# Performance work log

Measured on AMD Instinct MI355X. Metric: run time of the kernel, lower is better.

## Reference

```python
import jax, jax.numpy as jnp
import numpy as np
from jax import lax

B, T, D = 8, 2048, 1024


def setup_inputs() -> dict:
    key = jax.random.key(0)
    ks = jax.random.split(key, 8)
    s = 1.0 / np.sqrt(D)
    x = jax.random.normal(ks[0], (B, T, D), dtype=jnp.float32)
    Wq = jax.random.uniform(ks[1], (D, D), jnp.float32, -s, s)
    bq = jax.random.uniform(ks[2], (D,), jnp.float32, -s, s)
    Wk = jax.random.uniform(ks[3], (D, D), jnp.float32, -s, s)
    bk = jax.random.uniform(ks[4], (D,), jnp.float32, -s, s)
    Wv = jax.random.uniform(ks[5], (D, D), jnp.float32, -s, s)
    bv = jax.random.uniform(ks[6], (D,), jnp.float32, -s, s)
    decay = jnp.full((D,), 0.9, dtype=jnp.float32)  # nn.Parameter(ones*0.9)
    return {"x": x, "Wq": Wq, "bq": bq, "Wk": Wk, "bk": bk,
            "Wv": Wv, "bv": bv, "decay": decay}


def reference(x, Wq, bq, Wk, bk, Wv, bv, decay):
    # projections (torch Linear: x @ W.T + b)
    q = jnp.einsum('btd,ed->bte', x, Wq) + bq
    k = jnp.einsum('btd,ed->bte', x, Wk) + bk
    v = jnp.einsum('btd,ed->bte', x, Wv) + bv
    kv = k * v  # [B,T,D]

    # diagonal-decay linear recurrence: mem_t = decay * mem_{t-1} + kv_t
    def step(mem, kv_t):
        mem = decay * mem + kv_t  # [B,D]
        return mem, mem

    mem0 = jnp.zeros((B, D), dtype=x.dtype)
    _, mems = lax.scan(step, mem0, jnp.swapaxes(kv, 0, 1))  # mems: [T,B,D]
    out = q * jnp.swapaxes(mems, 0, 1)  # output_t = q_t * mem_t
    return out
```

## Files before the change

### kernel.cpp

```cpp
#include <hip/hip_runtime.h>
#include <cstdint>

typedef unsigned short ushort_t;
typedef __bf16 bf16x8 __attribute__((ext_vector_type(8)));
typedef float f32x4 __attribute__((ext_vector_type(4)));

#define B_ 8
#define T_ 2048
#define D_ 1024
#define M_ (B_ * T_)
#define NCHUNK 64
#define CHUNKLEN 32

__device__ __forceinline__ ushort_t f2bf(float f) {
    union { float f; uint32_t u; } v; v.f = f;
    uint32_t u = v.u;
    uint32_t r = (u + 0x7fffu + ((u >> 16) & 1u)) >> 16;
    return (ushort_t)r;
}
__device__ __forceinline__ float bf2f(ushort_t h) {
    union { uint32_t u; float f; } v; v.u = ((uint32_t)h) << 16;
    return v.f;
}

__device__ __forceinline__ void async16(const ushort_t* g, ushort_t* l) {
    __builtin_amdgcn_global_load_lds(
        (const __attribute__((address_space(1))) void*)g,
        (__attribute__((address_space(3))) void*)l, 16, 0, 0);
}

__global__ __launch_bounds__(256) void cast_all(
    const float* __restrict__ x, const float* __restrict__ wq,
    const float* __restrict__ wk, const float* __restrict__ wv,
    ushort_t* __restrict__ xb, ushort_t* __restrict__ Wb) {
    const int nx4 = M_ * D_ / 4, nw4 = D_ * D_ / 4;
    int i = blockIdx.x * blockDim.x + threadIdx.x;
    const float* src; ushort_t* dstp; int si;
    if (i < nx4) {
        src = x; si = i; dstp = xb + (size_t)i * 4;
    } else {
        int j = i - nx4;
        dstp = Wb + (size_t)j * 4;
        if (j < nw4)          { src = wq; si = j; }
        else if (j < 2 * nw4) { src = wk; si = j - nw4; }
        else                  { src = wv; si = j - 2 * nw4; }
    }
    float4 v = ((const float4*)src)[si];
    ushort4 o;
    o.x = f2bf(v.x); o.y = f2bf(v.y); o.z = f2bf(v.z); o.w = f2bf(v.w);
    *(ushort4*)dstp = o;
}

__global__ __launch_bounds__(256, 2) void gemm_qkv(
    const ushort_t* __restrict__ xb, const ushort_t* __restrict__ Wq,
    const ushort_t* __restrict__ Wk, const ushort_t* __restrict__ Wv,
    const float* __restrict__ bq, const float* __restrict__ bk,
    const float* __restrict__ bv, const float* __restrict__ decay,
    ushort_t* __restrict__ qb, ushort_t* __restrict__ kvb,
    float* __restrict__ S) {
    __shared__ ushort_t As[128 * 64];
    __shared__ ushort_t B0[128 * 64];
    __shared__ ushort_t B1[128 * 64];

    const int idx = blockIdx.x;
    const bool qmode = idx < 512;
    int mb, n0;
    const ushort_t *W0, *W1;
    if (qmode) {
        mb = idx & 127; n0 = (idx >> 7) * 256;
        W0 = Wq + (size_t)n0 * D_;
        W1 = Wq + (size_t)(n0 + 128) * D_;
    } else {
        const int j = idx - 512;
        mb = j & 127; n0 = (j >> 7) * 128;
        W0 = Wk + (size_t)n0 * D_;
        W1 = Wv + (size_t)n0 * D_;
    }
    const int m0 = mb * 128;

    const int t = threadIdx.x;
    const int lane = t & 63, wv = t >> 6;
    const int wr = (wv >> 1) * 64, wc = (wv & 1) * 64;

    f32x4 acc0[4][4], acc1[4][4];
#pragma unroll
    for (int i = 0; i < 4; ++i)
#pragma unroll
        for (int j = 0; j < 4; ++j) {
            acc0[i][j] = (f32x4){0.f, 0.f, 0.f, 0.f};
            acc1[i][j] = (f32x4){0.f, 0.f, 0.f, 0.f};
        }

    const int rs = t >> 3;
    const int g = (t & 7) ^ (rs & 7);
    const int scol = g * 8;

    const int quad = lane >> 4;
    const int l7 = lane & 7;
    const int cs0 = ((quad) ^ l7) * 8;
    const int cs1 = ((4 + quad) ^ l7) * 8;
    const int rowa = wr + (lane & 15);
    const int rowb = wc + (lane & 15);

    for (int kt = 0; kt < 16; ++kt) {
        const int k0 = kt * 64;
#pragma unroll
        for (int p = 0; p < 4; ++p) {
            const int rp = rs + p * 32;
            const int Lofs = (t + p * 256) * 8;
            async16(xb + (size_t)(m0 + rp) * D_ + k0 + scol, &As[Lofs]);
            async16(W0 + (size_t)rp * D_ + k0 + scol, &B0[Lofs]);
            async16(W1 + (size_t)rp * D_ + k0 + scol, &B1[Lofs]);
        }
        __syncthreads();

#pragma unroll
        for (int h = 0; h < 2; ++h) {
            const int cs = h ? cs1 : cs0;
            bf16x8 af[4], b08[4], b18[4];
#pragma unroll
            for (int i = 0; i < 4; ++i)
                af[i] = *(const bf16x8*)&As[(rowa + i * 16) * 64 + cs];
#pragma unroll
            for (int j = 0; j < 4; ++j) {
                b08[j] = *(const bf16x8*)&B0[(rowb + j * 16) * 64 + cs];
                b18[j] = *(const bf16x8*)&B1[(rowb + j * 16) * 64 + cs];
            }
#pragma unroll
            for (int i = 0; i < 4; ++i)
#pragma unroll
                for (int j = 0; j < 4; ++j) {
                    acc0[i][j] = __builtin_amdgcn_mfma_f32_16x16x32_bf16(
                        af[i], b08[j], acc0[i][j], 0, 0, 0);
                    acc1[i][j] = __builtin_amdgcn_mfma_f32_16x16x32_bf16(
                        af[i], b18[j], acc1[i][j], 0, 0, 0);
                }
        }
        __syncthreads();
    }

    const int colq = lane & 15;
    const int rowq = quad * 4;

    if (qmode) {
        const float* bias0 = bq + n0;
        const float* bias1 = bq + n0 + 128;
#pragma unroll
        for (int i = 0; i < 4; ++i) {
#pragma unroll
            for (int j = 0; j < 4; ++j) {
                const int c = wc + j * 16 + colq;
                const float bv0 = bias0[c], bv1 = bias1[c];
#pragma unroll
                for (int r = 0; r < 4; ++r) {
                    const int rg = m0 + wr + i * 16 + rowq + r;
                    qb[(size_t)rg * D_ + n0 + c]       = f2bf(acc0[i][j][r] + bv0);
                    qb[(size_t)rg * D_ + n0 + 128 + c] = f2bf(acc1[i][j][r] + bv1);
                }
            }
        }
    } else {
        const float* bias0 = bk + n0;
        const float* bias1 = bv + n0;
        const int bidx = m0 >> 11;
        const int cbase = ((m0 & 2047) >> 5) + (wr >> 5);
        int cj[4];
        float bv0a[4], bv1a[4], d1a[4], d2a[4], d3a[4], P0a[4], P1a[4];
#pragma unroll
        for (int j = 0; j < 4; ++j) {
            const int c = wc + j * 16 + colq;
            cj[j] = c;
            bv0a[j] = bias0[c];
            bv1a[j] = bias1[c];
            const float dec = decay[n0 + c];
            const float d2 = dec * dec, d4 = d2 * d2;
            const float d8 = d4 * d4, d16 = d8 * d8;
            d1a[j] = dec; d2a[j] = d2; d3a[j] = d2 * dec;
            const float P1 = (quad == 0) ? (d8 * d4) : ((quad == 1) ? d8 : ((quad == 2) ? d4 : 1.0f));
            P1a[j] = P1;
            P0a[j] = d16 * P1;
        }
        float s0[4], s1[4];
#pragma unroll
        for (int j = 0; j < 4; ++j) { s0[j] = 0.f; s1[j] = 0.f; }

#pragma unroll
        for (int i = 0; i < 4; ++i) {
#pragma unroll
            for (int r = 0; r < 4; ++r) {
                const int rg = m0 + wr + i * 16 + rowq + r;
                ushort_t* rowp = kvb + (size_t)rg * D_ + n0;
#pragma unroll
                for (int j = 0; j < 4; ++j) {
                    const float kf = acc0[i][j][r] + bv0a[j];
                    const float vf = acc1[i][j][r] + bv1a[j];
                    const float kvf = kf * vf;
                    rowp[cj[j]] = f2bf(kvf);
                    const float w3 = (r == 0) ? d3a[j] : ((r == 1) ? d2a[j] : ((r == 2) ? d1a[j] : 1.0f));
                    const float wgt = ((i & 1) ? P1a[j] : P0a[j]) * w3;
                    if (i < 2) s0[j] = fmaf(kvf, wgt, s0[j]);
                    else       s1[j] = fmaf(kvf, wgt, s1[j]);
                }
            }
        }
#pragma unroll
        for (int j = 0; j < 4; ++j) {
            s0[j] += __shfl_xor(s0[j], 16, 64);
            s0[j] += __shfl_xor(s0[j], 32, 64);
            s1[j] += __shfl_xor(s1[j], 16, 64);
            s1[j] += __shfl_xor(s1[j], 32, 64);
        }
        if (quad == 0) {
#pragma unroll
            for (int j = 0; j < 4; ++j) {
                const int cg = n0 + cj[j];
                S[(((size_t)bidx * NCHUNK) + cbase) * D_ + cg]     = s0[j];
                S[(((size_t)bidx * NCHUNK) + cbase + 1) * D_ + cg] = s1[j];
            }
        }
    }
}

__global__ __launch_bounds__(256) void scan_final2(
    const ushort_t* __restrict__ kvb, const ushort_t* __restrict__ qb,
    const float* __restrict__ decay, const float* __restrict__ S,
    float* __restrict__ out) {
    const int b = blockIdx.x >> 6;
    const int c = blockIdx.x & 63;
    const int d0 = threadIdx.x * 4;
    const float4 dc = *(const float4*)&decay[d0];
    float e0 = dc.x, e1 = dc.y, e2 = dc.z, e3 = dc.w;
#pragma unroll
    for (int s = 0; s < 5; ++s) { e0 *= e0; e1 *= e1; e2 *= e2; e3 *= e3; }
    float m0 = 0.f, m1 = 0.f, m2 = 0.f, m3 = 0.f;
    const float* Sb = &S[((size_t)b * NCHUNK) * D_ + d0];
    for (int cc = 0; cc < c; ++cc) {
        float4 s4 = *(const float4*)&Sb[(size_t)cc * D_];
        m0 = fmaf(e0, m0, s4.x);
        m1 = fmaf(e1, m1, s4.y);
        m2 = fmaf(e2, m2, s4.z);
        m3 = fmaf(e3, m3, s4.w);
    }
    size_t base = ((size_t)b * T_ + c * CHUNKLEN) * D_ + d0;
#pragma unroll 8
    for (int i = 0; i < CHUNKLEN; ++i) {
        const size_t o = base + (size_t)i * D_;
        ushort4 kv = *(const ushort4*)&kvb[o];
        ushort4 q4 = *(const ushort4*)&qb[o];
        m0 = fmaf(dc.x, m0, bf2f(kv.x));
        m1 = fmaf(dc.y, m1, bf2f(kv.y));
        m2 = fmaf(dc.z, m2, bf2f(kv.z));
        m3 = fmaf(dc.w, m3, bf2f(kv.w));
        *(float4*)&out[o] = make_float4(bf2f(q4.x) * m0, bf2f(q4.y) * m1,
                                        bf2f(q4.z) * m2, bf2f(q4.w) * m3);
    }
}

extern "C" void kernel_launch(void* const* d_in, const int* in_sizes, int n_in,
                              void* d_out, int out_size, void* d_ws, size_t ws_size,
                              hipStream_t stream) {
    const float* x     = (const float*)d_in[0];
    const float* Wq    = (const float*)d_in[1];
    const float* bq    = (const float*)d_in[2];
    const float* Wk    = (const float*)d_in[3];
    const float* bk    = (const float*)d_in[4];
    const float* Wv    = (const float*)d_in[5];
    const float* bv    = (const float*)d_in[6];
    const float* decay = (const float*)d_in[7];
    float* out = (float*)d_out;

    char* ws = (char*)d_ws;
    ushort_t* xb  = (ushort_t*)(ws);
    ushort_t* Wb  = (ushort_t*)(ws + 33554432);
    ushort_t* qb  = (ushort_t*)(ws + 39845888);
    ushort_t* kvb = (ushort_t*)(ws + 73400320);
    float*    S   = (float*)(ws + 106954752);

    ushort_t* Wqb = Wb;
    ushort_t* Wkb = Wb + D_ * D_;
    ushort_t* Wvb = Wb + 2 * D_ * D_;

    const int ncast = (M_ * D_ / 4) + (3 * D_ * D_ / 4);
    cast_all<<<ncast / 256, 256, 0, stream>>>(x, Wq, Wk, Wv, xb, Wb);

    gemm_qkv<<<1536, 256, 0, stream>>>(xb, Wqb, Wkb, Wvb, bq, bk, bv, decay,
                                       qb, kvb, S);

    scan_final2<<<B_ * NCHUNK, 256, 0, stream>>>(kvb, qb, decay, S, out);
}
```

Baseline: 257.3 us.

## Double-buffer GEMM LDS tiles with K=32 stages and split scan over more blocks

The QKV GEMM now uses two LDS buffers of K=32 tiles, issuing async loads for the next tile while MFMAs run on the current one. This hides global-to-LDS latency and drops one barrier per step, with a new swizzle for the narrower rows. The final scan kernel splits D across two blocks per (batch, chunk), doubling the grid to 1024 blocks with 2 elements per thread. That raises occupancy and parallelism for the memory-bound output pass, at the cost of narrower vector accesses.

Measured after the change: 302.0 us. 17.4% more time.

```diff
diff --git a/kernel.cpp b/kernel.cpp
--- a/kernel.cpp
+++ b/kernel.cpp
@@ -58,9 +58,9 @@
     const float* __restrict__ bv, const float* __restrict__ decay,
     ushort_t* __restrict__ qb, ushort_t* __restrict__ kvb,
     float* __restrict__ S) {
-    __shared__ ushort_t As[128 * 64];
-    __shared__ ushort_t B0[128 * 64];
-    __shared__ ushort_t B1[128 * 64];
+    __shared__ ushort_t As[2][128 * 32];
+    __shared__ ushort_t B0[2][128 * 32];
+    __shared__ ushort_t B1[2][128 * 32];
 
     const int idx = blockIdx.x;
     const bool qmode = idx < 512;
@@ -91,53 +91,58 @@
             acc1[i][j] = (f32x4){0.f, 0.f, 0.f, 0.f};
         }
 
-    const int rs = t >> 3;
-    const int g = (t & 7) ^ (rs & 7);
+    const int rs = t >> 2;
+    const int g = (t & 3) ^ ((t >> 3) & 3);
     const int scol = g * 8;
 
     const int quad = lane >> 4;
-    const int l7 = lane & 7;
-    const int cs0 = ((quad) ^ l7) * 8;
-    const int cs1 = ((4 + quad) ^ l7) * 8;
+    const int rsw = ((lane & 15) >> 1) & 3;
+    const int cs = (quad ^ rsw) * 8;
     const int rowa = wr + (lane & 15);
     const int rowb = wc + (lane & 15);
 
-    for (int kt = 0; kt < 16; ++kt) {
-        const int k0 = kt * 64;
-#pragma unroll
-        for (int p = 0; p < 4; ++p) {
-            const int rp = rs + p * 32;
-            const int Lofs = (t + p * 256) * 8;
-            async16(xb + (size_t)(m0 + rp) * D_ + k0 + scol, &As[Lofs]);
-            async16(W0 + (size_t)rp * D_ + k0 + scol, &B0[Lofs]);
-            async16(W1 + (size_t)rp * D_ + k0 + scol, &B1[Lofs]);
-        }
+#define STAGE(bufi, ktv)                                                     \
+    do {                                                                     \
+        const int k0s = (ktv) * 32;                                          \
+        _Pragma("unroll")                                                    \
+        for (int p = 0; p < 2; ++p) {                                        \
+            const int rp = rs + p * 64;                                      \
+            const int Lofs = (t + p * 256) * 8;                              \
+            async16(xb + (size_t)(m0 + rp) * D_ + k0s + scol,                \
+                    &As[bufi][Lofs]);                                        \
+            async16(W0 + (size_t)rp * D_ + k0s + scol, &B0[bufi][Lofs]);     \
+            async16(W1 + (size_t)rp * D_ + k0s + scol, &B1[bufi][Lofs]);     \
+        }                                                                    \
+    } while (0)
+
+    STAGE(0, 0);
+    __syncthreads();
+
+    for (int kt = 0; kt < 32; ++kt) {
+        const int cur = kt & 1;
+        if (kt < 31) STAGE(cur ^ 1, kt + 1);
+
+        bf16x8 af[4], b08[4], b18[4];
+#pragma unroll
+        for (int i = 0; i < 4; ++i)
+            af[i] = *(const bf16x8*)&As[cur][(rowa + i * 16) * 32 + cs];
+#pragma unroll
+        for (int j = 0; j < 4; ++j) {
+            b08[j] = *(const bf16x8*)&B0[cur][(rowb + j * 16) * 32 + cs];
+            b18[j] = *(const bf16x8*)&B1[cur][(rowb + j * 16) * 32 + cs];
+        }
+#pragma unroll
+        for (int i = 0; i < 4; ++i)
+#pragma unroll
+            for (int j = 0; j < 4; ++j) {
+                acc0[i][j] = __builtin_amdgcn_mfma_f32_16x16x32_bf16(
+                    af[i], b08[j], acc0[i][j], 0, 0, 0);
+                acc1[i][j] = __builtin_amdgcn_mfma_f32_16x16x32_bf16(
+                    af[i], b18[j], acc1[i][j], 0, 0, 0);
+            }
         __syncthreads();
-
-#pragma unroll
-        for (int h = 0; h < 2; ++h) {
-            const int cs = h ? cs1 : cs0;
-            bf16x8 af[4], b08[4], b18[4];
-#pragma unroll
-            for (int i = 0; i < 4; ++i)
-                af[i] = *(const bf16x8*)&As[(rowa + i * 16) * 64 + cs];
-#pragma unroll
-            for (int j = 0; j < 4; ++j) {
-                b08[j] = *(const bf16x8*)&B0[(rowb + j * 16) * 64 + cs];
-                b18[j] = *(const bf16x8*)&B1[(rowb + j * 16) * 64 + cs];
-            }
-#pragma unroll
-            for (int i = 0; i < 4; ++i)
-#pragma unroll
-                for (int j = 0; j < 4; ++j) {
-                    acc0[i][j] = __builtin_amdgcn_mfma_f32_16x16x32_bf16(
-                        af[i], b08[j], acc0[i][j], 0, 0, 0);
-                    acc1[i][j] = __builtin_amdgcn_mfma_f32_16x16x32_bf16(
-                        af[i], b18[j], acc1[i][j], 0, 0, 0);
-                }
-        }
-        __syncthreads();
-    }
+    }
+#undef STAGE
 
     const int colq = lane & 15;
     const int rowq = quad * 4;
@@ -225,34 +230,31 @@
     const ushort_t* __restrict__ kvb, const ushort_t* __restrict__ qb,
     const float* __restrict__ decay, const float* __restrict__ S,
     float* __restrict__ out) {
-    const int b = blockIdx.x >> 6;
-    const int c = blockIdx.x & 63;
-    const int d0 = threadIdx.x * 4;
-    const float4 dc = *(const float4*)&decay[d0];
-    float e0 = dc.x, e1 = dc.y, e2 = dc.z, e3 = dc.w;
-#pragma unroll
-    for (int s = 0; s < 5; ++s) { e0 *= e0; e1 *= e1; e2 *= e2; e3 *= e3; }
-    float m0 = 0.f, m1 = 0.f, m2 = 0.f, m3 = 0.f;
+    const int bid = blockIdx.x;
+    const int b = bid >> 7;
+    const int c = (bid >> 1) & 63;
+    const int dh = bid & 1;
+    const int d0 = dh * 512 + threadIdx.x * 2;
+    const float2 dc2 = *(const float2*)&decay[d0];
+    float e0 = dc2.x, e1 = dc2.y;
+#pragma unroll
+    for (int s = 0; s < 5; ++s) { e0 *= e0; e1 *= e1; }
+    float m0 = 0.f, m1 = 0.f;
     const float* Sb = &S[((size_t)b * NCHUNK) * D_ + d0];
     for (int cc = 0; cc < c; ++cc) {
-        float4 s4 = *(const float4*)&Sb[(size_t)cc * D_];
-        m0 = fmaf(e0, m0, s4.x);
-        m1 = fmaf(e1, m1, s4.y);
-        m2 = fmaf(e2, m2, s4.z);
-        m3 = fmaf(e3, m3, s4.w);
+        const float2 s2 = *(const float2*)&Sb[(size_t)cc * D_];
+        m0 = fmaf(e0, m0, s2.x);
+        m1 = fmaf(e1, m1, s2.y);
     }
     size_t base = ((size_t)b * T_ + c * CHUNKLEN) * D_ + d0;
 #pragma unroll 8
     for (int i = 0; i < CHUNKLEN; ++i) {
         const size_t o = base + (size_t)i * D_;
-        ushort4 kv = *(const ushort4*)&kvb[o];
-        ushort4 q4 = *(const ushort4*)&qb[o];
-        m0 = fmaf(dc.x, m0, bf2f(kv.x));
-        m1 = fmaf(dc.y, m1, bf2f(kv.y));
-        m2 = fmaf(dc.z, m2, bf2f(kv.z));
-        m3 = fmaf(dc.w, m3, bf2f(kv.w));
-        *(float4*)&out[o] = make_float4(bf2f(q4.x) * m0, bf2f(q4.y) * m1,
-                                        bf2f(q4.z) * m2, bf2f(q4.w) * m3);
+        const ushort2 kv = *(const ushort2*)&kvb[o];
+        const ushort2 q2 = *(const ushort2*)&qb[o];
+        m0 = fmaf(dc2.x, m0, bf2f(kv.x));
+        m1 = fmaf(dc2.y, m1, bf2f(kv.y));
+        *(float2*)&out[o] = make_float2(bf2f(q2.x) * m0, bf2f(q2.y) * m1);
     }
 }
 
@@ -286,5 +288,5 @@
     gemm_qkv<<<1536, 256, 0, stream>>>(xb, Wqb, Wkb, Wvb, bq, bk, bv, decay,
                                        qb, kvb, S);
 
-    scan_final2<<<B_ * NCHUNK, 256, 0, stream>>>(kvb, qb, decay, S, out);
-}
+    scan_final2<<<B_ * NCHUNK * 2, 256, 0, stream>>>(kvb, qb, decay, S, out);
+}
```
